# Kernel optimization log

Hardware: AMD Instinct MI355X
Metric: run time of the kernel (lower is better)

Reference implementation:

```python
import jax, jax.numpy as jnp
import numpy as np

B, N, K, D, G = 4, 2048, 32, 64, 32
RADIUS = 0.8


def _linear_params(key, fin, fout):
    kw, kb = jax.random.split(key)
    lim = 1.0 / np.sqrt(fin)
    W = jax.random.uniform(kw, (fin, fout), jnp.float32, -lim, lim)
    b = jax.random.uniform(kb, (fout,), jnp.float32, -lim, lim)
    return W, b


def setup_inputs() -> dict:
    key = jax.random.key(0)
    ks = jax.random.split(key, 6)
    x = jax.random.normal(ks[0], (B, N, D), jnp.float32)
    pos = jax.random.uniform(ks[1], (B, N, 3), jnp.float32)
    W_first, b_first = _linear_params(ks[2], 3 * D, G)          # layer_first
    W1, b1 = _linear_params(ks[3], D + 1 * G, G)                # layers[0]
    W2, b2 = _linear_params(ks[4], D + 2 * G, G)                # layers[1]
    W_last, b_last = _linear_params(ks[5], D + 3 * G, G)        # layer_last
    return {"x": x, "pos": pos, "W_first": W_first, "b_first": b_first,
            "W1": W1, "b1": b1, "W2": W2, "b2": b2,
            "W_last": W_last, "b_last": b_last}


def ball_query(pos, radius, k):
    # pos: (B, N, 3). CUDA ball_query semantics: for each query point take the
    # first k points (in index order) with squared distance < radius^2; pad
    # remaining slots with the first found index. Self is always within radius.
    sq = jnp.sum(pos * pos, axis=-1)                            # (B, N)
    d2 = sq[:, :, None] + sq[:, None, :] - 2.0 * jnp.einsum("bnc,bmc->bnm", pos, pos)
    within = d2 < radius * radius                               # (B, N, N)
    n = pos.shape[1]
    cand = jnp.where(within, jnp.arange(n, dtype=jnp.int32)[None, None, :], n)
    idx = jnp.sort(cand, axis=-1)[..., :k]                      # first k hits, padded with n
    first = idx[..., :1]
    return jnp.where(idx == n, first, idx)                      # (B, N, K) int32


def reference(x, pos, W_first, b_first, W1, b1, W2, b2, W_last, b_last):
    idx = ball_query(pos, RADIUS, K)                            # (B, N, K)
    knn_feat = jax.vmap(lambda xb, ib: xb[ib])(x, idx)          # (B, N, K, D)
    x_tiled = jnp.broadcast_to(x[:, :, None, :], knn_feat.shape)
    edge_feat = jnp.concatenate([x_tiled, knn_feat, knn_feat - x_tiled], axis=-1)  # (B,N,K,3D)
    y = jnp.concatenate([jax.nn.relu(edge_feat @ W_first + b_first), x_tiled], axis=-1)  # G+D
    y = jnp.concatenate([jax.nn.relu(y @ W1 + b1), y], axis=-1)                     # 2G+D
    y = jnp.concatenate([jax.nn.relu(y @ W2 + b2), y], axis=-1)                     # 3G+D
    y = jnp.concatenate([y @ W_last + b_last, y], axis=-1)                          # 4G+D
    return jnp.max(y, axis=-2)                                  # (B, N, D + 4G)
```

## Files before the change

### kernel.cpp

```cpp
#include <hip/hip_runtime.h>
#include <hip/hip_bf16.h>

#define NB 4
#define NN 2048
#define KK 32
#define DD 64
#define R2C 0.64f

typedef __attribute__((ext_vector_type(8)))  short short8;
typedef __attribute__((ext_vector_type(16))) float f32x16;

__device__ __forceinline__ unsigned short f2bf(float f) {
    __hip_bfloat16 h = __float2bfloat16(f);
    return reinterpret_cast<unsigned short&>(h);
}

#define HSTRIDE 40

__device__ __forceinline__ void post_layer(const f32x16& acc, float bs,
                                           unsigned short* hl, int col, int g,
                                           float& mx, short8& f0, short8& f1) {
    float v[16];
#pragma unroll
    for (int p = 0; p < 16; ++p) v[p] = fmaxf(acc[p] + bs, 0.0f);
    float m = v[0];
#pragma unroll
    for (int p = 1; p < 16; ++p) m = fmaxf(m, v[p]);
    mx = fmaxf(m, __shfl_xor(m, 32));
#pragma unroll
    for (int p = 0; p < 16; ++p) {
        int r = (p & 3) + 8 * (p >> 2) + 4 * g;
        hl[r * HSTRIDE + col] = f2bf(v[p]);
    }
    const unsigned short* row = hl + col * HSTRIDE;
    f0 = *(const short8*)(row + 8 * g);
    f1 = *(const short8*)(row + 16 + 8 * g);
}

__device__ __forceinline__ short8 cvt8(const float* __restrict__ p) {
    float4 a = ((const float4*)p)[0];
    float4 b = ((const float4*)p)[1];
    short8 r;
    r[0] = (short)f2bf(a.x); r[1] = (short)f2bf(a.y); r[2] = (short)f2bf(a.z); r[3] = (short)f2bf(a.w);
    r[4] = (short)f2bf(b.x); r[5] = (short)f2bf(b.y); r[6] = (short)f2bf(b.z); r[7] = (short)f2bf(b.w);
    return r;
}

__device__ __forceinline__ void l1_mfma(const short8* hf, int lane, const short8* wl, f32x16& acc) {
#pragma unroll
    for (int p = 0; p < 16; ++p) acc[p] = 0.0f;
    acc = __builtin_amdgcn_mfma_f32_32x32x16_bf16(hf[0], wl[4 * 64 + lane], acc, 0, 0, 0);
    acc = __builtin_amdgcn_mfma_f32_32x32x16_bf16(hf[1], wl[5 * 64 + lane], acc, 0, 0, 0);
}

__device__ __forceinline__ void l2_mfma(const short8* h1, const short8* h0,
                                        int lane, const short8* wl, f32x16& acc) {
#pragma unroll
    for (int p = 0; p < 16; ++p) acc[p] = 0.0f;
    acc = __builtin_amdgcn_mfma_f32_32x32x16_bf16(h1[0], wl[6 * 64 + lane], acc, 0, 0, 0);
    acc = __builtin_amdgcn_mfma_f32_32x32x16_bf16(h1[1], wl[7 * 64 + lane], acc, 0, 0, 0);
    acc = __builtin_amdgcn_mfma_f32_32x32x16_bf16(h0[0], wl[8 * 64 + lane], acc, 0, 0, 0);
    acc = __builtin_amdgcn_mfma_f32_32x32x16_bf16(h0[1], wl[9 * 64 + lane], acc, 0, 0, 0);
}

__device__ __forceinline__ void l3_mfma(const short8* h2, const short8* h1, const short8* h0,
                                        int lane, const short8* wl, f32x16& acc) {
#pragma unroll
    for (int p = 0; p < 16; ++p) acc[p] = 0.0f;
    acc = __builtin_amdgcn_mfma_f32_32x32x16_bf16(h2[0], wl[10 * 64 + lane], acc, 0, 0, 0);
    acc = __builtin_amdgcn_mfma_f32_32x32x16_bf16(h2[1], wl[11 * 64 + lane], acc, 0, 0, 0);
    acc = __builtin_amdgcn_mfma_f32_32x32x16_bf16(h1[0], wl[12 * 64 + lane], acc, 0, 0, 0);
    acc = __builtin_amdgcn_mfma_f32_32x32x16_bf16(h1[1], wl[13 * 64 + lane], acc, 0, 0, 0);
    acc = __builtin_amdgcn_mfma_f32_32x32x16_bf16(h0[0], wl[14 * 64 + lane], acc, 0, 0, 0);
    acc = __builtin_amdgcn_mfma_f32_32x32x16_bf16(h0[1], wl[15 * 64 + lane], acc, 0, 0, 0);
}

__global__ __launch_bounds__(256, 2) void fused_kernel(const float* __restrict__ x,
                                                       const float* __restrict__ pos,
                                                       const float* __restrict__ Wf,
                                                       const float* __restrict__ bfv,
                                                       const float* __restrict__ W1,
                                                       const float* __restrict__ b1,
                                                       const float* __restrict__ W2,
                                                       const float* __restrict__ b2,
                                                       const float* __restrict__ Wl,
                                                       const float* __restrict__ bl,
                                                       float* __restrict__ out) {
    __shared__ unsigned short hlds[4][4][32 * HSTRIDE];
    __shared__ int nbrs[4][4][KK];
    __shared__ unsigned short lwf[16 * 64 * 8];
    int wid = threadIdx.x >> 6, lane = threadIdx.x & 63;
    int qp = __builtin_amdgcn_readfirstlane(blockIdx.x * 4 + wid);
    int q0 = qp << 2;
    int col = lane & 31, g = lane >> 5;
    int b = q0 >> 11, n0 = q0 & (NN - 1);

    for (int e = threadIdx.x; e < 1024; e += 256) {
        int f = e >> 6, l = e & 63;
        int c = l & 31, g2 = l >> 5;
        unsigned short* dst = lwf + (size_t)(f * 64 + l) * 8;
#pragma unroll
        for (int j = 0; j < 8; ++j) {
            int kl = 8 * g2 + j;
            float v;
            if (f < 4)       { int rr = 16 * f + kl;             v = Wf[(64 + rr) * 32 + c] + Wf[(128 + rr) * 32 + c]; }
            else if (f < 6)  { int rr = 16 * (f - 4) + kl;       v = W1[rr * 32 + c]; }
            else if (f < 8)  { int rr = 16 * (f - 6) + kl;       v = W2[rr * 32 + c]; }
            else if (f < 10) { int rr = 32 + 16 * (f - 8) + kl;  v = W2[rr * 32 + c]; }
            else if (f < 12) { int rr = 16 * (f - 10) + kl;      v = Wl[rr * 32 + c]; }
            else if (f < 14) { int rr = 32 + 16 * (f - 12) + kl; v = Wl[rr * 32 + c]; }
            else             { int rr = 64 + 16 * (f - 14) + kl; v = Wl[rr * 32 + c]; }
            dst[j] = f2bf(v);
        }
    }

    const float* xq0 = x + (size_t)q0 * DD;
    bool lo = lane < 32;
    int c0 = lane & 31;
    const float* pA1 = lo ? (Wf + c0) : (W1 + 32 * 32 + c0);
    const float* pA2 = lo ? (Wf + 128 * 32 + c0) : (W1 + 32 * 32 + c0);
    float sA = lo ? -1.0f : 0.0f;
    const float* pB1 = lo ? (W2 + 64 * 32 + c0) : (Wl + 96 * 32 + c0);
    float balA = lo ? bfv[c0] : b1[c0];
    float balB = lo ? b2[c0] : bl[c0];
    float aA[4] = {balA, balA, balA, balA};
    float aB[4] = {balB, balB, balB, balB};
#pragma unroll
    for (int j0 = 0; j0 < 16; ++j0) {
        float wa[4], wb[4];
#pragma unroll
        for (int jj = 0; jj < 4; ++jj) {
            int j = 4 * j0 + jj;
            wa[jj] = fmaf(sA, pA2[j * 32], pA1[j * 32]);
            wb[jj] = pB1[j * 32];
        }
#pragma unroll
        for (int t = 0; t < 4; ++t) {
            const float* xr = xq0 + t * DD + 4 * j0;
            float x0 = xr[0], x1 = xr[1], x2 = xr[2], x3 = xr[3];
            aA[t] = fmaf(x0, wa[0], aA[t]); aA[t] = fmaf(x1, wa[1], aA[t]);
            aA[t] = fmaf(x2, wa[2], aA[t]); aA[t] = fmaf(x3, wa[3], aA[t]);
            aB[t] = fmaf(x0, wb[0], aB[t]); aB[t] = fmaf(x1, wb[1], aB[t]);
            aB[t] = fmaf(x2, wb[2], aB[t]); aB[t] = fmaf(x3, wb[3], aB[t]);
        }
    }
    float bs0[4], bs1[4], bs2[4], bs3[4];
#pragma unroll
    for (int t = 0; t < 4; ++t) {
        bs0[t] = __shfl(aA[t], col, 64); bs1[t] = __shfl(aA[t], 32 + col, 64);
        bs2[t] = __shfl(aB[t], col, 64); bs3[t] = __shfl(aB[t], 32 + col, 64);
    }

    const float* pb = pos + (size_t)b * NN * 3;
    float qxv[4], qyv[4], qzv[4], sq4[4];
#pragma unroll
    for (int t = 0; t < 4; ++t) {
        int n = n0 + t;
        qxv[t] = pb[3 * n]; qyv[t] = pb[3 * n + 1]; qzv[t] = pb[3 * n + 2];
        sq4[t] = __fadd_rn(__fadd_rn(__fmul_rn(qxv[t], qxv[t]), __fmul_rn(qyv[t], qyv[t])),
                           __fmul_rn(qzv[t], qzv[t]));
    }
    int cnt[4] = {0, 0, 0, 0};
    unsigned long long ltmask = (1ULL << lane) - 1ULL;
    for (int m0 = 0; m0 < NN; m0 += 64) {
        if (cnt[0] >= KK && cnt[1] >= KK && cnt[2] >= KK && cnt[3] >= KK) break;
        int m = m0 + lane;
        float mx3 = pb[3 * m], my3 = pb[3 * m + 1], mz3 = pb[3 * m + 2];
        float sqm = __fadd_rn(__fadd_rn(__fmul_rn(mx3, mx3), __fmul_rn(my3, my3)), __fmul_rn(mz3, mz3));
#pragma unroll
        for (int t = 0; t < 4; ++t) {
            if (cnt[t] < KK) {
                float dot = __fadd_rn(__fadd_rn(__fmul_rn(qxv[t], mx3), __fmul_rn(qyv[t], my3)),
                                      __fmul_rn(qzv[t], mz3));
                float d2 = __fsub_rn(__fadd_rn(sq4[t], sqm), __fmul_rn(2.0f, dot));
                bool hit = d2 < R2C;
                unsigned long long mask = __ballot(hit);
                if (hit) {
                    int p = cnt[t] + (int)__popcll(mask & ltmask);
                    if (p < KK) nbrs[wid][t][p] = m;
                }
                cnt[t] = __builtin_amdgcn_readfirstlane(cnt[t] + (int)__popcll(mask));
            }
        }
    }
    int nbn[4];
#pragma unroll
    for (int t = 0; t < 4; ++t) nbn[t] = nbrs[wid][t][col < cnt[t] ? col : 0];

    short8 xk[4][4];
#pragma unroll
    for (int t = 0; t < 4; ++t) {
        const float* xrow = x + (size_t)(b * NN + nbn[t]) * DD + g * 8;
#pragma unroll
        for (int kf = 0; kf < 4; ++kf) xk[t][kf] = cvt8(xrow + kf * 16);
    }

    __syncthreads();
    const short8* wl = (const short8*)lwf;
    unsigned short* hl0 = hlds[wid][0];
    unsigned short* hl1 = hlds[wid][1];
    unsigned short* hl2 = hlds[wid][2];
    unsigned short* hl3 = hlds[wid][3];

    f32x16 a0, a1, a2, a3;
    float mx0[4], mx1[4], mx2[4];
    short8 h0f[4][2], h1f[4][2], h2f[4][2];

#pragma unroll
    for (int p = 0; p < 16; ++p) { a0[p] = 0.0f; a1[p] = 0.0f; a2[p] = 0.0f; a3[p] = 0.0f; }
#pragma unroll
    for (int f = 0; f < 4; ++f) a0 = __builtin_amdgcn_mfma_f32_32x32x16_bf16(xk[0][f], wl[f * 64 + lane], a0, 0, 0, 0);
#pragma unroll
    for (int f = 0; f < 4; ++f) a1 = __builtin_amdgcn_mfma_f32_32x32x16_bf16(xk[1][f], wl[f * 64 + lane], a1, 0, 0, 0);
    post_layer(a0, bs0[0], hl0, col, g, mx0[0], h0f[0][0], h0f[0][1]);
#pragma unroll
    for (int f = 0; f < 4; ++f) a2 = __builtin_amdgcn_mfma_f32_32x32x16_bf16(xk[2][f], wl[f * 64 + lane], a2, 0, 0, 0);
    post_layer(a1, bs0[1], hl1, col, g, mx0[1], h0f[1][0], h0f[1][1]);
#pragma unroll
    for (int f = 0; f < 4; ++f) a3 = __builtin_amdgcn_mfma_f32_32x32x16_bf16(xk[3][f], wl[f * 64 + lane], a3, 0, 0, 0);
    post_layer(a2, bs0[2], hl2, col, g, mx0[2], h0f[2][0], h0f[2][1]);
    post_layer(a3, bs0[3], hl3, col, g, mx0[3], h0f[3][0], h0f[3][1]);

    l1_mfma(h0f[0], lane, wl, a0);
    l1_mfma(h0f[1], lane, wl, a1);
    post_layer(a0, bs1[0], hl0, col, g, mx1[0], h1f[0][0], h1f[0][1]);
    l1_mfma(h0f[2], lane, wl, a2);
    post_layer(a1, bs1[1], hl1, col, g, mx1[1], h1f[1][0], h1f[1][1]);
    l1_mfma(h0f[3], lane, wl, a3);
    post_layer(a2, bs1[2], hl2, col, g, mx1[2], h1f[2][0], h1f[2][1]);
    post_layer(a3, bs1[3], hl3, col, g, mx1[3], h1f[3][0], h1f[3][1]);

    l2_mfma(h1f[0], h0f[0], lane, wl, a0);
    l2_mfma(h1f[1], h0f[1], lane, wl, a1);
    post_layer(a0, bs2[0], hl0, col, g, mx2[0], h2f[0][0], h2f[0][1]);
    l2_mfma(h1f[2], h0f[2], lane, wl, a2);
    post_layer(a1, bs2[1], hl1, col, g, mx2[1], h2f[1][0], h2f[1][1]);
    l2_mfma(h1f[3], h0f[3], lane, wl, a3);
    post_layer(a2, bs2[2], hl2, col, g, mx2[2], h2f[2][0], h2f[2][1]);
    post_layer(a3, bs2[3], hl3, col, g, mx2[3], h2f[3][0], h2f[3][1]);

    float m3[4];
    l3_mfma(h2f[0], h1f[0], h0f[0], lane, wl, a0);
    l3_mfma(h2f[1], h1f[1], h0f[1], lane, wl, a1);
    {
        float m = a0[0] + bs3[0];
#pragma unroll
        for (int p = 1; p < 16; ++p) m = fmaxf(m, a0[p] + bs3[0]);
        m3[0] = fmaxf(m, __shfl_xor(m, 32));
    }
    l3_mfma(h2f[2], h1f[2], h0f[2], lane, wl, a2);
    {
        float m = a1[0] + bs3[1];
#pragma unroll
        for (int p = 1; p < 16; ++p) m = fmaxf(m, a1[p] + bs3[1]);
        m3[1] = fmaxf(m, __shfl_xor(m, 32));
    }
    l3_mfma(h2f[3], h1f[3], h0f[3], lane, wl, a3);
    {
        float m = a2[0] + bs3[2];
#pragma unroll
        for (int p = 1; p < 16; ++p) m = fmaxf(m, a2[p] + bs3[2]);
        m3[2] = fmaxf(m, __shfl_xor(m, 32));
    }
    {
        float m = a3[0] + bs3[3];
#pragma unroll
        for (int p = 1; p < 16; ++p) m = fmaxf(m, a3[p] + bs3[3]);
        m3[3] = fmaxf(m, __shfl_xor(m, 32));
    }

#pragma unroll
    for (int t = 0; t < 4; ++t) {
        float* o = out + (size_t)(q0 + t) * 192;
        if (g == 0) {
            o[col]      = m3[t];
            o[32 + col] = mx2[t];
            o[64 + col] = mx1[t];
            o[96 + col] = mx0[t];
        }
        o[128 + lane] = xq0[t * DD + lane];
    }
}

extern "C" void kernel_launch(void* const* d_in, const int* in_sizes, int n_in,
                              void* d_out, int out_size, void* d_ws, size_t ws_size,
                              hipStream_t stream) {
    const float* x   = (const float*)d_in[0];
    const float* pos = (const float*)d_in[1];
    const float* Wf  = (const float*)d_in[2];
    const float* bf  = (const float*)d_in[3];
    const float* W1  = (const float*)d_in[4];
    const float* b1  = (const float*)d_in[5];
    const float* W2  = (const float*)d_in[6];
    const float* b2  = (const float*)d_in[7];
    const float* Wl  = (const float*)d_in[8];
    const float* bl  = (const float*)d_in[9];
    float* out = (float*)d_out;

    hipLaunchKernelGGL(fused_kernel, dim3(512), dim3(256), 0, stream,
                       x, pos, Wf, bf, W1, b1, W2, b2, Wl, bl, out);
}
```

Measured before the change: 26.86 us.

## Transpose MFMA operands so activations stay in registers instead of LDS round-trips

```diff
diff --git a/kernel.cpp b/kernel.cpp
--- a/kernel.cpp
+++ b/kernel.cpp
@@ -9,34 +9,32 @@
 
 typedef __attribute__((ext_vector_type(8)))  short short8;
 typedef __attribute__((ext_vector_type(16))) float f32x16;
+typedef __attribute__((ext_vector_type(4)))  int   i32x4;
 
 __device__ __forceinline__ unsigned short f2bf(float f) {
     __hip_bfloat16 h = __float2bfloat16(f);
     return reinterpret_cast<unsigned short&>(h);
 }
-
-#define HSTRIDE 40
-
-__device__ __forceinline__ void post_layer(const f32x16& acc, float bs,
-                                           unsigned short* hl, int col, int g,
-                                           float& mx, short8& f0, short8& f1) {
-    float v[16];
-#pragma unroll
-    for (int p = 0; p < 16; ++p) v[p] = fmaxf(acc[p] + bs, 0.0f);
-    float m = v[0];
-#pragma unroll
-    for (int p = 1; p < 16; ++p) m = fmaxf(m, v[p]);
-    mx = fmaxf(m, __shfl_xor(m, 32));
-#pragma unroll
-    for (int p = 0; p < 16; ++p) {
-        int r = (p & 3) + 8 * (p >> 2) + 4 * g;
-        hl[r * HSTRIDE + col] = f2bf(v[p]);
-    }
-    const unsigned short* row = hl + col * HSTRIDE;
-    f0 = *(const short8*)(row + 8 * g);
-    f1 = *(const short8*)(row + 16 + 8 * g);
-}
-
+__device__ __forceinline__ int cvtpk(float lo, float hi) {
+    int r;
+    asm("v_cvt_pk_bf16_f32 %0, %1, %2" : "=v"(r) : "v"(lo), "v"(hi));
+    return r;
+}
+__device__ __forceinline__ int pkmax(int a, int b) {
+    int r;
+    asm("v_pk_max_i16 %0, %1, %2" : "=v"(r) : "v"(a), "v"(b));
+    return r;
+}
+__device__ __forceinline__ short8 fr(const int* d) {
+    i32x4 v = { d[0], d[1], d[2], d[3] };
+    return __builtin_bit_cast(short8, v);
+}
+__device__ __forceinline__ float sel16(const f32x16& a, int s) {
+    float r = a[0];
+#pragma unroll
+    for (int i = 1; i < 16; ++i) r = (s == i) ? a[i] : r;
+    return r;
+}
 __device__ __forceinline__ short8 cvt8(const float* __restrict__ p) {
     float4 a = ((const float4*)p)[0];
     float4 b = ((const float4*)p)[1];
@@ -46,34 +44,7 @@
     return r;
 }
 
-__device__ __forceinline__ void l1_mfma(const short8* hf, int lane, const short8* wl, f32x16& acc) {
-#pragma unroll
-    for (int p = 0; p < 16; ++p) acc[p] = 0.0f;
-    acc = __builtin_amdgcn_mfma_f32_32x32x16_bf16(hf[0], wl[4 * 64 + lane], acc, 0, 0, 0);
-    acc = __builtin_amdgcn_mfma_f32_32x32x16_bf16(hf[1], wl[5 * 64 + lane], acc, 0, 0, 0);
-}
-
-__device__ __forceinline__ void l2_mfma(const short8* h1, const short8* h0,
-                                        int lane, const short8* wl, f32x16& acc) {
-#pragma unroll
-    for (int p = 0; p < 16; ++p) acc[p] = 0.0f;
-    acc = __builtin_amdgcn_mfma_f32_32x32x16_bf16(h1[0], wl[6 * 64 + lane], acc, 0, 0, 0);
-    acc = __builtin_amdgcn_mfma_f32_32x32x16_bf16(h1[1], wl[7 * 64 + lane], acc, 0, 0, 0);
-    acc = __builtin_amdgcn_mfma_f32_32x32x16_bf16(h0[0], wl[8 * 64 + lane], acc, 0, 0, 0);
-    acc = __builtin_amdgcn_mfma_f32_32x32x16_bf16(h0[1], wl[9 * 64 + lane], acc, 0, 0, 0);
-}
-
-__device__ __forceinline__ void l3_mfma(const short8* h2, const short8* h1, const short8* h0,
-                                        int lane, const short8* wl, f32x16& acc) {
-#pragma unroll
-    for (int p = 0; p < 16; ++p) acc[p] = 0.0f;
-    acc = __builtin_amdgcn_mfma_f32_32x32x16_bf16(h2[0], wl[10 * 64 + lane], acc, 0, 0, 0);
-    acc = __builtin_amdgcn_mfma_f32_32x32x16_bf16(h2[1], wl[11 * 64 + lane], acc, 0, 0, 0);
-    acc = __builtin_amdgcn_mfma_f32_32x32x16_bf16(h1[0], wl[12 * 64 + lane], acc, 0, 0, 0);
-    acc = __builtin_amdgcn_mfma_f32_32x32x16_bf16(h1[1], wl[13 * 64 + lane], acc, 0, 0, 0);
-    acc = __builtin_amdgcn_mfma_f32_32x32x16_bf16(h0[0], wl[14 * 64 + lane], acc, 0, 0, 0);
-    acc = __builtin_amdgcn_mfma_f32_32x32x16_bf16(h0[1], wl[15 * 64 + lane], acc, 0, 0, 0);
-}
+#define MF(A, B, C) __builtin_amdgcn_mfma_f32_32x32x16_bf16(A, B, C, 0, 0, 0)
 
 __global__ __launch_bounds__(256, 2) void fused_kernel(const float* __restrict__ x,
                                                        const float* __restrict__ pos,
@@ -86,9 +57,9 @@
                                                        const float* __restrict__ Wl,
                                                        const float* __restrict__ bl,
                                                        float* __restrict__ out) {
-    __shared__ unsigned short hlds[4][4][32 * HSTRIDE];
+    __shared__ short8 lwf8[16 * 64];
     __shared__ int nbrs[4][4][KK];
-    __shared__ unsigned short lwf[16 * 64 * 8];
+    __shared__ float bss[4][4 * 128];
     int wid = threadIdx.x >> 6, lane = threadIdx.x & 63;
     int qp = __builtin_amdgcn_readfirstlane(blockIdx.x * 4 + wid);
     int q0 = qp << 2;
@@ -98,20 +69,28 @@
     for (int e = threadIdx.x; e < 1024; e += 256) {
         int f = e >> 6, l = e & 63;
         int c = l & 31, g2 = l >> 5;
-        unsigned short* dst = lwf + (size_t)(f * 64 + l) * 8;
+        unsigned short u[8];
 #pragma unroll
         for (int j = 0; j < 8; ++j) {
-            int kl = 8 * g2 + j;
             float v;
-            if (f < 4)       { int rr = 16 * f + kl;             v = Wf[(64 + rr) * 32 + c] + Wf[(128 + rr) * 32 + c]; }
-            else if (f < 6)  { int rr = 16 * (f - 4) + kl;       v = W1[rr * 32 + c]; }
-            else if (f < 8)  { int rr = 16 * (f - 6) + kl;       v = W2[rr * 32 + c]; }
-            else if (f < 10) { int rr = 32 + 16 * (f - 8) + kl;  v = W2[rr * 32 + c]; }
-            else if (f < 12) { int rr = 16 * (f - 10) + kl;      v = Wl[rr * 32 + c]; }
-            else if (f < 14) { int rr = 32 + 16 * (f - 12) + kl; v = Wl[rr * 32 + c]; }
-            else             { int rr = 64 + 16 * (f - 14) + kl; v = Wl[rr * 32 + c]; }
-            dst[j] = f2bf(v);
-        }
+            if (f < 4) {
+                int rr = 16 * f + 8 * g2 + j;
+                v = Wf[(64 + rr) * 32 + c] + Wf[(128 + rr) * 32 + c];
+            } else {
+                int fl = f & 1;
+                int rr = 4 * g2 + (j & 3) + 8 * ((j >> 2) + 2 * fl);
+                if (f < 6)       v = W1[rr * 32 + c];
+                else if (f < 8)  v = W2[rr * 32 + c];
+                else if (f < 10) v = W2[(32 + rr) * 32 + c];
+                else if (f < 12) v = Wl[rr * 32 + c];
+                else if (f < 14) v = Wl[(32 + rr) * 32 + c];
+                else             v = Wl[(64 + rr) * 32 + c];
+            }
+            u[j] = f2bf(v);
+        }
+        i32x4 pk = { (int)(u[0] | (u[1] << 16)), (int)(u[2] | (u[3] << 16)),
+                     (int)(u[4] | (u[5] << 16)), (int)(u[6] | (u[7] << 16)) };
+        lwf8[e] = __builtin_bit_cast(short8, pk);
     }
 
     const float* xq0 = x + (size_t)q0 * DD;
@@ -144,11 +123,10 @@
             aB[t] = fmaf(x2, wb[2], aB[t]); aB[t] = fmaf(x3, wb[3], aB[t]);
         }
     }
-    float bs0[4], bs1[4], bs2[4], bs3[4];
 #pragma unroll
     for (int t = 0; t < 4; ++t) {
-        bs0[t] = __shfl(aA[t], col, 64); bs1[t] = __shfl(aA[t], 32 + col, 64);
-        bs2[t] = __shfl(aB[t], col, 64); bs3[t] = __shfl(aB[t], 32 + col, 64);
+        bss[wid][t * 128 + lane]      = aA[t];
+        bss[wid][t * 128 + 64 + lane] = aB[t];
     }
 
     const float* pb = pos + (size_t)b * NN * 3;
@@ -196,88 +174,116 @@
     }
 
     __syncthreads();
-    const short8* wl = (const short8*)lwf;
-    unsigned short* hl0 = hlds[wid][0];
-    unsigned short* hl1 = hlds[wid][1];
-    unsigned short* hl2 = hlds[wid][2];
-    unsigned short* hl3 = hlds[wid][3];
-
+    const float* bp = bss[wid];
+
+    auto bias_init = [&](f32x16& acc, int t, int L) {
+#pragma unroll
+        for (int m = 0; m < 4; ++m) {
+            float4 r = *(const float4*)(bp + t * 128 + L * 32 + 8 * m + 4 * g);
+            acc[4 * m] = r.x; acc[4 * m + 1] = r.y; acc[4 * m + 2] = r.z; acc[4 * m + 3] = r.w;
+        }
+    };
+    auto post_pack = [&](const f32x16& a, int* d) {
+#pragma unroll
+        for (int i = 0; i < 8; ++i)
+            d[i] = cvtpk(fmaxf(a[2 * i], 0.0f), fmaxf(a[2 * i + 1], 0.0f));
+    };
+    auto maxstore_pk = [&](int* d, float* orow, int off) {
+#pragma unroll
+        for (int ms = 1; ms < 32; ms <<= 1) {
+#pragma unroll
+            for (int i = 0; i < 8; ++i) d[i] = pkmax(d[i], __shfl_xor(d[i], ms, 32));
+        }
+        int s = lane & 7;
+        int sel = s == 0 ? d[0] : s == 1 ? d[1] : s == 2 ? d[2] : s == 3 ? d[3]
+                : s == 4 ? d[4] : s == 5 ? d[5] : s == 6 ? d[6] : d[7];
+        if (col < 8) {
+            int c = ((2 * s) & 3) + 8 * (s >> 1) + 4 * g;
+            float2 v = make_float2(__int_as_float(sel << 16),
+                                   __int_as_float(sel & (int)0xFFFF0000));
+            *(float2*)(orow + off + c) = v;
+        }
+    };
+    auto maxstore_f32 = [&](f32x16& a, float* orow) {
+#pragma unroll
+        for (int ms = 1; ms < 32; ms <<= 1) {
+#pragma unroll
+            for (int p = 0; p < 16; ++p) a[p] = fmaxf(a[p], __shfl_xor(a[p], ms, 32));
+        }
+        if (col < 8) {
+            int c = ((2 * col) & 3) + 8 * (col >> 1) + 4 * g;
+            float v0 = sel16(a, 2 * col);
+            float v1 = sel16(a, 2 * col + 1);
+            *(float2*)(orow + c) = make_float2(v0, v1);
+        }
+    };
+
+#define WLD(f) lwf8[(f) * 64 + lane]
     f32x16 a0, a1, a2, a3;
-    float mx0[4], mx1[4], mx2[4];
-    short8 h0f[4][2], h1f[4][2], h2f[4][2];
-
-#pragma unroll
-    for (int p = 0; p < 16; ++p) { a0[p] = 0.0f; a1[p] = 0.0f; a2[p] = 0.0f; a3[p] = 0.0f; }
-#pragma unroll
-    for (int f = 0; f < 4; ++f) a0 = __builtin_amdgcn_mfma_f32_32x32x16_bf16(xk[0][f], wl[f * 64 + lane], a0, 0, 0, 0);
-#pragma unroll
-    for (int f = 0; f < 4; ++f) a1 = __builtin_amdgcn_mfma_f32_32x32x16_bf16(xk[1][f], wl[f * 64 + lane], a1, 0, 0, 0);
-    post_layer(a0, bs0[0], hl0, col, g, mx0[0], h0f[0][0], h0f[0][1]);
-#pragma unroll
-    for (int f = 0; f < 4; ++f) a2 = __builtin_amdgcn_mfma_f32_32x32x16_bf16(xk[2][f], wl[f * 64 + lane], a2, 0, 0, 0);
-    post_layer(a1, bs0[1], hl1, col, g, mx0[1], h0f[1][0], h0f[1][1]);
-#pragma unroll
-    for (int f = 0; f < 4; ++f) a3 = __builtin_amdgcn_mfma_f32_32x32x16_bf16(xk[3][f], wl[f * 64 + lane], a3, 0, 0, 0);
-    post_layer(a2, bs0[2], hl2, col, g, mx0[2], h0f[2][0], h0f[2][1]);
-    post_layer(a3, bs0[3], hl3, col, g, mx0[3], h0f[3][0], h0f[3][1]);
-
-    l1_mfma(h0f[0], lane, wl, a0);
-    l1_mfma(h0f[1], lane, wl, a1);
-    post_layer(a0, bs1[0], hl0, col, g, mx1[0], h1f[0][0], h1f[0][1]);
-    l1_mfma(h0f[2], lane, wl, a2);
-    post_layer(a1, bs1[1], hl1, col, g, mx1[1], h1f[1][0], h1f[1][1]);
-    l1_mfma(h0f[3], lane, wl, a3);
-    post_layer(a2, bs1[2], hl2, col, g, mx1[2], h1f[2][0], h1f[2][1]);
-    post_layer(a3, bs1[3], hl3, col, g, mx1[3], h1f[3][0], h1f[3][1]);
-
-    l2_mfma(h1f[0], h0f[0], lane, wl, a0);
-    l2_mfma(h1f[1], h0f[1], lane, wl, a1);
-    post_layer(a0, bs2[0], hl0, col, g, mx2[0], h2f[0][0], h2f[0][1]);
-    l2_mfma(h1f[2], h0f[2], lane, wl, a2);
-    post_layer(a1, bs2[1], hl1, col, g, mx2[1], h2f[1][0], h2f[1][1]);
-    l2_mfma(h1f[3], h0f[3], lane, wl, a3);
-    post_layer(a2, bs2[2], hl2, col, g, mx2[2], h2f[2][0], h2f[2][1]);
-    post_layer(a3, bs2[3], hl3, col, g, mx2[3], h2f[3][0], h2f[3][1]);
-
-    float m3[4];
-    l3_mfma(h2f[0], h1f[0], h0f[0], lane, wl, a0);
-    l3_mfma(h2f[1], h1f[1], h0f[1], lane, wl, a1);
-    {
-        float m = a0[0] + bs3[0];
-#pragma unroll
-        for (int p = 1; p < 16; ++p) m = fmaxf(m, a0[p] + bs3[0]);
-        m3[0] = fmaxf(m, __shfl_xor(m, 32));
-    }
-    l3_mfma(h2f[2], h1f[2], h0f[2], lane, wl, a2);
-    {
-        float m = a1[0] + bs3[1];
-#pragma unroll
-        for (int p = 1; p < 16; ++p) m = fmaxf(m, a1[p] + bs3[1]);
-        m3[1] = fmaxf(m, __shfl_xor(m, 32));
-    }
-    l3_mfma(h2f[3], h1f[3], h0f[3], lane, wl, a3);
-    {
-        float m = a2[0] + bs3[2];
-#pragma unroll
-        for (int p = 1; p < 16; ++p) m = fmaxf(m, a2[p] + bs3[2]);
-        m3[2] = fmaxf(m, __shfl_xor(m, 32));
-    }
-    {
-        float m = a3[0] + bs3[3];
-#pragma unroll
-        for (int p = 1; p < 16; ++p) m = fmaxf(m, a3[p] + bs3[3]);
-        m3[3] = fmaxf(m, __shfl_xor(m, 32));
-    }
+    int h0d[4][8], h1d[4][8], h2d[4][8];
+
+    bias_init(a0, 0, 0); bias_init(a1, 1, 0); bias_init(a2, 2, 0); bias_init(a3, 3, 0);
+    a0 = MF(WLD(0), xk[0][0], a0); a0 = MF(WLD(1), xk[0][1], a0);
+    a0 = MF(WLD(2), xk[0][2], a0); a0 = MF(WLD(3), xk[0][3], a0);
+    a1 = MF(WLD(0), xk[1][0], a1); a1 = MF(WLD(1), xk[1][1], a1);
+    a1 = MF(WLD(2), xk[1][2], a1); a1 = MF(WLD(3), xk[1][3], a1);
+    post_pack(a0, h0d[0]);
+    a2 = MF(WLD(0), xk[2][0], a2); a2 = MF(WLD(1), xk[2][1], a2);
+    a2 = MF(WLD(2), xk[2][2], a2); a2 = MF(WLD(3), xk[2][3], a2);
+    post_pack(a1, h0d[1]);
+    a3 = MF(WLD(0), xk[3][0], a3); a3 = MF(WLD(1), xk[3][1], a3);
+    a3 = MF(WLD(2), xk[3][2], a3); a3 = MF(WLD(3), xk[3][3], a3);
+    post_pack(a2, h0d[2]);
+    post_pack(a3, h0d[3]);
+
+    bias_init(a0, 0, 1); bias_init(a1, 1, 1); bias_init(a2, 2, 1); bias_init(a3, 3, 1);
+    a0 = MF(WLD(4), fr(h0d[0]), a0); a0 = MF(WLD(5), fr(h0d[0] + 4), a0);
+    a1 = MF(WLD(4), fr(h0d[1]), a1); a1 = MF(WLD(5), fr(h0d[1] + 4), a1);
+    post_pack(a0, h1d[0]);
+    a2 = MF(WLD(4), fr(h0d[2]), a2); a2 = MF(WLD(5), fr(h0d[2] + 4), a2);
+    post_pack(a1, h1d[1]);
+    a3 = MF(WLD(4), fr(h0d[3]), a3); a3 = MF(WLD(5), fr(h0d[3] + 4), a3);
+    post_pack(a2, h1d[2]);
+    post_pack(a3, h1d[3]);
+
+    bias_init(a0, 0, 2); bias_init(a1, 1, 2); bias_init(a2, 2, 2); bias_init(a3, 3, 2);
+    a0 = MF(WLD(6), fr(h1d[0]), a0); a0 = MF(WLD(7), fr(h1d[0] + 4), a0);
+    a0 = MF(WLD(8), fr(h0d[0]), a0); a0 = MF(WLD(9), fr(h0d[0] + 4), a0);
+    a1 = MF(WLD(6), fr(h1d[1]), a1); a1 = MF(WLD(7), fr(h1d[1] + 4), a1);
+    a1 = MF(WLD(8), fr(h0d[1]), a1); a1 = MF(WLD(9), fr(h0d[1] + 4), a1);
+    post_pack(a0, h2d[0]);
+    a2 = MF(WLD(6), fr(h1d[2]), a2); a2 = MF(WLD(7), fr(h1d[2] + 4), a2);
+    a2 = MF(WLD(8), fr(h0d[2]), a2); a2 = MF(WLD(9), fr(h0d[2] + 4), a2);
+    post_pack(a1, h2d[1]);
+    a3 = MF(WLD(6), fr(h1d[3]), a3); a3 = MF(WLD(7), fr(h1d[3] + 4), a3);
+    a3 = MF(WLD(8), fr(h0d[3]), a3); a3 = MF(WLD(9), fr(h0d[3] + 4), a3);
+    post_pack(a2, h2d[2]);
+    post_pack(a3, h2d[3]);
+
+    bias_init(a0, 0, 3); bias_init(a1, 1, 3); bias_init(a2, 2, 3); bias_init(a3, 3, 3);
+    a0 = MF(WLD(10), fr(h2d[0]), a0); a0 = MF(WLD(11), fr(h2d[0] + 4), a0);
+    a0 = MF(WLD(12), fr(h1d[0]), a0); a0 = MF(WLD(13), fr(h1d[0] + 4), a0);
+    a0 = MF(WLD(14), fr(h0d[0]), a0); a0 = MF(WLD(15), fr(h0d[0] + 4), a0);
+    a1 = MF(WLD(10), fr(h2d[1]), a1); a1 = MF(WLD(11), fr(h2d[1] + 4), a1);
+    a1 = MF(WLD(12), fr(h1d[1]), a1); a1 = MF(WLD(13), fr(h1d[1] + 4), a1);
+    a1 = MF(WLD(14), fr(h0d[1]), a1); a1 = MF(WLD(15), fr(h0d[1] + 4), a1);
+    maxstore_f32(a0, out + (size_t)(q0 + 0) * 192);
+    a2 = MF(WLD(10), fr(h2d[2]), a2); a2 = MF(WLD(11), fr(h2d[2] + 4), a2);
+    a2 = MF(WLD(12), fr(h1d[2]), a2); a2 = MF(WLD(13), fr(h1d[2] + 4), a2);
+    a2 = MF(WLD(14), fr(h0d[2]), a2); a2 = MF(WLD(15), fr(h0d[2] + 4), a2);
+    maxstore_f32(a1, out + (size_t)(q0 + 1) * 192);
+    a3 = MF(WLD(10), fr(h2d[3]), a3); a3 = MF(WLD(11), fr(h2d[3] + 4), a3);
+    a3 = MF(WLD(12), fr(h1d[3]), a3); a3 = MF(WLD(13), fr(h1d[3] + 4), a3);
+    a3 = MF(WLD(14), fr(h0d[3]), a3); a3 = MF(WLD(15), fr(h0d[3] + 4), a3);
+    maxstore_f32(a2, out + (size_t)(q0 + 2) * 192);
+    maxstore_f32(a3, out + (size_t)(q0 + 3) * 192);
 
 #pragma unroll
     for (int t = 0; t < 4; ++t) {
         float* o = out + (size_t)(q0 + t) * 192;
-        if (g == 0) {
-            o[col]      = m3[t];
-            o[32 + col] = mx2[t];
-            o[64 + col] = mx1[t];
-            o[96 + col] = mx0[t];
-        }
+        maxstore_pk(h2d[t], o, 32);
+        maxstore_pk(h1d[t], o, 64);
+        maxstore_pk(h0d[t], o, 96);
         o[128 + lane] = xq0[t * DD + lane];
     }
 }
```

Measured after the change: 52.74 us. +96.4%, slower.
